# Optimization experiments

Hardware: AMD Instinct MI355X
Metric: run time of the kernel (lower is better)

The kernel has to match this reference:

```python
import jax, jax.numpy as jnp
import numpy as np

B, L, D, H = 4, 2048, 1024, 16
HD = D // H
EPS = 1e-5


def _layernorm(x, g, b):
    mu = jnp.mean(x, axis=-1, keepdims=True)
    var = jnp.mean(jnp.square(x - mu), axis=-1, keepdims=True)
    return (x - mu) * jax.lax.rsqrt(var + EPS) * g + b


def _rotate_half(x):
    x1, x2 = jnp.split(x, 2, axis=-1)
    return jnp.concatenate([-x2, x1], axis=-1)


def setup_inputs() -> dict:
    key = jax.random.key(0)
    ks = jax.random.split(key, 12)
    s = 0.02
    return {
        "x": jax.random.normal(ks[0], (B, L, D), jnp.float32),
        "pos_cos": jax.random.uniform(ks[1], (B, L, D), jnp.float32),
        "pos_sin": jax.random.uniform(ks[2], (B, L, D), jnp.float32),
        "attn_mask": jnp.zeros((B, L), jnp.float32),
        "Wq": jax.random.normal(ks[3], (D, D), jnp.float32) * s,
        "Wk": jax.random.normal(ks[4], (D, D), jnp.float32) * s,
        "Wv": jax.random.normal(ks[5], (D, D), jnp.float32) * s,
        "Wo": jax.random.normal(ks[6], (D, D), jnp.float32) * s,
        "W1": jax.random.normal(ks[7], (D, 2 * D), jnp.float32) * s,
        "W2": jax.random.normal(ks[8], (D, D), jnp.float32) * s,
        "g1": jnp.ones((D,), jnp.float32),
        "b1": jnp.zeros((D,), jnp.float32),
        "g2": jnp.ones((D,), jnp.float32),
        "b2": jnp.zeros((D,), jnp.float32),
    }


def reference(x, pos_cos, pos_sin, attn_mask, Wq, Wk, Wv, Wo, W1, W2, g1, b1, g2, b2):
    # --- attention sublayer (pre-LN) ---
    residual = x
    xn = _layernorm(x, g1, b1)
    split_heads = lambda t: t.reshape(B, L, H, HD).transpose(0, 2, 1, 3)  # [B,H,L,hd]
    q = split_heads(xn @ Wq)
    k = split_heads(xn @ Wk)
    v = split_heads(xn @ Wv)
    cos = split_heads(pos_cos)
    sin = split_heads(pos_sin)
    q = q * cos + _rotate_half(q) * sin
    k = k * cos + _rotate_half(k) * sin
    scores = jnp.einsum('bhqd,bhkd->bhqk', q, k) / np.float32(np.sqrt(HD))
    scores = scores + attn_mask[:, None, None, :]  # additive mask over keys
    probs = jax.nn.softmax(scores, axis=-1)
    ctx = jnp.einsum('bhqk,bhkd->bhqd', probs, v)
    ctx = ctx.transpose(0, 2, 1, 3).reshape(B, L, D)
    x = residual + ctx @ Wo
    # --- SwiGLU FFN sublayer (pre-LN) ---
    residual = x
    xn = _layernorm(x, g2, b2)
    h = xn @ W1
    x1, x2 = h[..., :D], h[..., D:]
    ffn = (jax.nn.silu(x1) * x2) @ W2
    return residual + ffn
```

## Files before the change

### kernel.cpp

```cpp
#include <hip/hip_runtime.h>
#include <hip/hip_bf16.h>

typedef unsigned short ushort_t;
typedef short short8 __attribute__((ext_vector_type(8)));
typedef unsigned short u16x4 __attribute__((ext_vector_type(4)));
typedef float f32x4 __attribute__((ext_vector_type(4)));
typedef int int2v __attribute__((ext_vector_type(2)));
typedef int int4v __attribute__((ext_vector_type(4)));

#define MFMA_BF16 __builtin_amdgcn_mfma_f32_16x16x32_bf16

#define GLDS16(g, l) __builtin_amdgcn_global_load_lds( \
    (__attribute__((address_space(1))) void*)(g), \
    (__attribute__((address_space(3))) void*)(l), 16, 0, 0)

__device__ __forceinline__ unsigned short f2bf(float f) {
  union { float f; unsigned u; } v; v.f = f;
  unsigned r = v.u + 0x7FFFu + ((v.u >> 16) & 1u);
  return (unsigned short)(r >> 16);
}
__device__ __forceinline__ float bf2f(unsigned short h) {
  union { unsigned u; float f; } v; v.u = ((unsigned)h) << 16;
  return v.f;
}
__device__ __forceinline__ unsigned pack_bf2(float a, float b) {
  __hip_bfloat162 t = __float22bfloat162_rn(float2{a, b});
  union { __hip_bfloat162 h; unsigned u; } v; v.h = t;
  return v.u;
}
__device__ __forceinline__ float exp2_raw(float x) {
  float r;
  asm volatile("v_exp_f32 %0, %1" : "=v"(r) : "v"(x));
  return r;
}

#define BB 4
#define LL 2048
#define DD 1024
#define HH 16
#define HD 64
#define NROW (BB * LL)
#define LOG2E 1.4426950408889634f

template <int PERM>
__global__ __launch_bounds__(256) void wconv(const float* __restrict__ W,
                                             ushort_t* __restrict__ WT,
                                             int R, int C) {
  __shared__ float tile[32][33];
  const int ct = blockIdx.x * 32, rt = blockIdx.y * 32;
  const int tx = threadIdx.x & 31, ty = threadIdx.x >> 5;
#pragma unroll
  for (int j = 0; j < 4; ++j)
    tile[ty + j * 8][tx] = W[(size_t)(rt + ty + j * 8) * C + ct + tx];
  __syncthreads();
  int orow0 = ct;
  if (PERM)
    orow0 = (ct < 1024) ? ((ct >> 5) * 64) : ((((ct - 1024) >> 5) * 64) + 32);
#pragma unroll
  for (int j = 0; j < 4; ++j)
    WT[(size_t)(orow0 + ty + j * 8) * R + rt + tx] = f2bf(tile[tx][ty + j * 8]);
}

__global__ void mask_scale(const float* __restrict__ mask,
                           float* __restrict__ maskl) {
  const int i = blockIdx.x * 256 + threadIdx.x;
  maskl[i] = mask[i] * LOG2E;
}

template <int BIN>
__global__ __launch_bounds__(256) void ln_kernel(const void* __restrict__ xin,
                                                 const float* __restrict__ g,
                                                 const float* __restrict__ bt,
                                                 ushort_t* __restrict__ out,
                                                 ushort_t* __restrict__ xb) {
  const int row = blockIdx.x, t = threadIdx.x;
  f32x4 v;
  if (BIN) {
    const u16x4 hv =
        *(const u16x4*)((const ushort_t*)xin + (size_t)row * DD + t * 4);
    v[0] = bf2f(hv[0]); v[1] = bf2f(hv[1]);
    v[2] = bf2f(hv[2]); v[3] = bf2f(hv[3]);
  } else {
    v = *(const f32x4*)((const float*)xin + (size_t)row * DD + t * 4);
    if (xb) {
      u16x4 xo;
      xo[0] = f2bf(v[0]); xo[1] = f2bf(v[1]);
      xo[2] = f2bf(v[2]); xo[3] = f2bf(v[3]);
      *(u16x4*)(xb + (size_t)row * DD + t * 4) = xo;
    }
  }
  float s = v[0] + v[1] + v[2] + v[3];
  float sq = v[0] * v[0] + v[1] * v[1] + v[2] * v[2] + v[3] * v[3];
#pragma unroll
  for (int off = 1; off < 64; off <<= 1) {
    s += __shfl_xor(s, off);
    sq += __shfl_xor(sq, off);
  }
  __shared__ float aw[4], aq[4];
  if ((t & 63) == 0) { aw[t >> 6] = s; aq[t >> 6] = sq; }
  __syncthreads();
  s = aw[0] + aw[1] + aw[2] + aw[3];
  sq = aq[0] + aq[1] + aq[2] + aq[3];
  const float mu = s * (1.f / DD);
  const float var = sq * (1.f / DD) - mu * mu;
  const float rs = rsqrtf(var + 1e-5f);
  u16x4 o;
#pragma unroll
  for (int j = 0; j < 4; ++j) {
    const int c = t * 4 + j;
    o[j] = f2bf((v[j] - mu) * rs * g[c] + bt[c]);
  }
  *(u16x4*)(out + (size_t)row * DD + t * 4) = o;
}

template <int EPI>
__global__ __launch_bounds__(256) void gemm64(
    const ushort_t* __restrict__ A, const ushort_t* __restrict__ BT,
    const float* __restrict__ pcos, const float* __restrict__ psin,
    ushort_t* __restrict__ qh, ushort_t* __restrict__ kh,
    ushort_t* __restrict__ vt, ushort_t* __restrict__ gact,
    ushort_t* __restrict__ Cb, float* __restrict__ Cf,
    const ushort_t* __restrict__ residb,
    int M, int N, int K) {
  __shared__ ushort_t As[2][128 * 64];
  __shared__ ushort_t Bs[2][128 * 64];
  const int tid = threadIdx.x;
  const int lane = tid & 63;
  const int w = tid >> 6;
  const int wr = w >> 1, wc = w & 1;
  const int orig = blockIdx.y * gridDim.x + blockIdx.x;
  const int xcd = orig & 7;
  const int lid = orig >> 3;
  const int bm = (xcd * 8 + (lid & 7)) * 128;
  const int bn = (lid >> 3) * 128;
  const int fr = lane & 15;
  const int hi = lane >> 4;
  const int srow8 = lane >> 3;
  const int schunk = (lane & 7) ^ srow8;
  f32x4 acc[4][4];
#pragma unroll
  for (int m = 0; m < 4; ++m)
#pragma unroll
    for (int n = 0; n < 4; ++n) acc[m][n] = (f32x4){0.f, 0.f, 0.f, 0.f};

#define STAGE64(kt, bb)                                                      \
  {                                                                          \
    _Pragma("unroll") for (int c = 0; c < 4; ++c) {                          \
      const int rbase = w * 32 + c * 8;                                      \
      const int grow = rbase + srow8;                                        \
      GLDS16(A + (size_t)(bm + grow) * K + (kt) * 64 + schunk * 8,           \
             &As[bb][rbase * 64]);                                           \
      GLDS16(BT + (size_t)(bn + grow) * K + (kt) * 64 + schunk * 8,          \
             &Bs[bb][rbase * 64]);                                           \
    }                                                                        \
  }

  const int nk = K >> 6;
  STAGE64(0, 0);
#pragma unroll 1
  for (int kt = 0; kt < nk; ++kt) {
    const int cur = kt & 1;
    if (kt + 1 < nk) {
      STAGE64(kt + 1, cur ^ 1);
      asm volatile("s_waitcnt vmcnt(8)" ::: "memory");
    } else {
      asm volatile("s_waitcnt vmcnt(0)" ::: "memory");
    }
    __syncthreads();
#pragma unroll
    for (int khf = 0; khf < 2; ++khf) {
      short8 af[4], bf_[4];
#pragma unroll
      for (int m = 0; m < 4; ++m) {
        const int r = wr * 64 + m * 16 + fr;
        af[m] =
            *(const short8*)&As[cur][r * 64 + (((khf << 2) + hi) ^ (fr & 7)) * 8];
      }
#pragma unroll
      for (int n = 0; n < 4; ++n) {
        const int r = wc * 64 + n * 16 + fr;
        bf_[n] =
            *(const short8*)&Bs[cur][r * 64 + (((khf << 2) + hi) ^ (fr & 7)) * 8];
      }
      __builtin_amdgcn_s_setprio(1);
#pragma unroll
      for (int m = 0; m < 4; ++m)
#pragma unroll
        for (int n = 0; n < 4; ++n)
          acc[m][n] = MFMA_BF16(af[m], bf_[n], acc[m][n], 0, 0, 0);
      __builtin_amdgcn_s_setprio(0);
    }
    __syncthreads();
  }
#undef STAGE64

  if (EPI == 1) {
    const int gcol = bn + wc * 64;
    const int region = gcol >> 10;
    const int h = (gcol & 1023) >> 6;
    const int b = bm >> 11;
    if (region < 2) {
      const float qs = (region == 0) ? (0.125f * LOG2E) : 1.0f;
      ushort_t* dstbuf = (region == 0) ? qh : kh;
      const int dbase = h * 64;
#pragma unroll
      for (int m = 0; m < 4; ++m) {
        const int gr0 = bm + wr * 64 + m * 16 + hi * 4;
#pragma unroll
        for (int r = 0; r < 4; ++r) {
          const int gr = gr0 + r;
          const int l = gr & 2047;
          const float* pcr = pcos + (size_t)gr * DD + dbase;
          const float* psr = psin + (size_t)gr * DD + dbase;
          ushort_t* dst = dstbuf + ((size_t)(b * HH + h) * LL + l) * HD;
#pragma unroll
          for (int n = 0; n < 2; ++n) {
            const int dlo = n * 16 + fr;
            const float xlo = acc[m][n][r], xhi = acc[m][n + 2][r];
            dst[dlo] = f2bf((xlo * pcr[dlo] - xhi * psr[dlo]) * qs);
            dst[dlo + 32] = f2bf((xhi * pcr[dlo + 32] + xlo * psr[dlo + 32]) * qs);
          }
        }
      }
    } else {
      const size_t bhv = (size_t)(b * HH + h);
      const int l0 = (bm & 2047) + wr * 64;
      const int lt = l0 >> 6;
#pragma unroll
      for (int m = 0; m < 4; ++m) {
        const int slotb = 32 * (m >> 1) + 8 * hi + 4 * (m & 1);
#pragma unroll
        for (int n = 0; n < 4; ++n) {
          const int hd = n * 16 + fr;
          u16x4 wv;
          wv[0] = f2bf(acc[m][n][0]);
          wv[1] = f2bf(acc[m][n][1]);
          wv[2] = f2bf(acc[m][n][2]);
          wv[3] = f2bf(acc[m][n][3]);
          *(u16x4*)(vt + (bhv * HD + hd) * LL + lt * 64 + slotb) = wv;
        }
      }
    }
  } else if (EPI == 2) {
    const int jbase = ((bn + wc * 64) >> 6) * 32;
#pragma unroll
    for (int m = 0; m < 4; ++m) {
      const int gr0 = bm + wr * 64 + m * 16 + hi * 4;
#pragma unroll
      for (int r = 0; r < 4; ++r) {
        ushort_t* dst = gact + (size_t)(gr0 + r) * DD + jbase;
#pragma unroll
        for (int n = 0; n < 2; ++n) {
          const float x1 = acc[m][n][r];
          const float x2 = acc[m][n + 2][r];
          dst[n * 16 + fr] = f2bf(x1 / (1.f + __expf(-x1)) * x2);
        }
      }
    }
  } else {
#pragma unroll
    for (int m = 0; m < 4; ++m)
#pragma unroll
      for (int n = 0; n < 4; ++n)
#pragma unroll
        for (int r = 0; r < 4; ++r) {
          const int gr = bm + wr * 64 + m * 16 + hi * 4 + r;
          const int gc = bn + wc * 64 + n * 16 + fr;
          const size_t o = (size_t)gr * N + gc;
          if (EPI == 3) Cb[o] = f2bf(bf2f(residb[o]) + acc[m][n][r]);
          else          Cf[o] = bf2f(residb[o]) + acc[m][n][r];
        }
  }
}

__global__ __launch_bounds__(512) void attn_kernel(
    const ushort_t* __restrict__ qh, const ushort_t* __restrict__ kh,
    const ushort_t* __restrict__ vt, const float* __restrict__ maskl,
    ushort_t* __restrict__ ctx) {
  const int tid = threadIdx.x, lane = tid & 63, w = tid >> 6;
  const int flat = blockIdx.y * gridDim.x + blockIdx.x;
  const int xcd = flat & 7;
  const int slot = flat >> 3;
  const int bh = xcd * 8 + (slot >> 4);
  const int q0 = (slot & 15) * 128;
  const int b = bh >> 4, h = bh & 15;
  __shared__ ushort_t Ks[2][64 * 64];
  __shared__ ushort_t Vs[2][64 * 64];
  const int fr = lane & 15;
  const int hi = lane >> 4;
  const int fo = hi * 8;
  const int qrow = q0 + w * 16 + fr;
  const size_t qoff = ((size_t)bh * LL + qrow) * HD + fo;
  const short8 qf0 = *(const short8*)(qh + qoff);
  const short8 qf1 = *(const short8*)(qh + qoff + 32);
  short8 ones;
#pragma unroll
  for (int i = 0; i < 8; ++i) ones[i] = (short)0x3F80;

  f32x4 oacc[4];
  f32x4 lacc = (f32x4){0.f, 0.f, 0.f, 0.f};
#pragma unroll
  for (int m = 0; m < 4; ++m) oacc[m] = (f32x4){0.f, 0.f, 0.f, 0.f};

  const int lrow = lane >> 3;
  const int lcs = ((lane & 7) ^ lrow) * 8;
  const int rr = w * 8 + lrow;

  const float* mrow = maskl + (size_t)b * LL;

  const int NT = LL / 128;
  for (int kt = 0; kt < NT; ++kt) {
    __syncthreads();
    GLDS16(kh + ((size_t)bh * LL + kt * 128 + rr) * HD + lcs, &Ks[0][w * 512]);
    GLDS16(kh + ((size_t)bh * LL + kt * 128 + 64 + rr) * HD + lcs,
           &Ks[1][w * 512]);
    GLDS16(vt + ((size_t)bh * HD + rr) * LL + kt * 128 + lcs, &Vs[0][w * 512]);
    GLDS16(vt + ((size_t)bh * HD + rr) * LL + kt * 128 + 64 + lcs,
           &Vs[1][w * 512]);
    f32x4 mk[8];
#pragma unroll
    for (int n = 0; n < 8; ++n)
      mk[n] = *(const f32x4*)(mrow + kt * 128 + n * 16 + hi * 4);
    asm volatile("s_waitcnt vmcnt(0)" ::: "memory");
    __syncthreads();

#pragma unroll
    for (int sub = 0; sub < 2; ++sub) {
      f32x4 s[4];
#pragma unroll
      for (int n = 0; n < 4; ++n) s[n] = mk[sub * 4 + n];
      __builtin_amdgcn_s_setprio(1);
#pragma unroll
      for (int n = 0; n < 4; ++n) {
        const int krow = n * 16 + fr;
#pragma unroll
        for (int c = 0; c < 2; ++c) {
          const int col = (c * 32 + fo) ^ ((fr & 7) * 8);
          const short8 kf = *(const short8*)&Ks[sub][krow * 64 + col];
          s[n] = MFMA_BF16(kf, c ? qf1 : qf0, s[n], 0, 0, 0);
        }
      }
      __builtin_amdgcn_s_setprio(0);
      unsigned pk[4][2];
#pragma unroll
      for (int n = 0; n < 4; ++n) {
        const float p0 = exp2_raw(s[n][0]);
        const float p1 = exp2_raw(s[n][1]);
        const float p2 = exp2_raw(s[n][2]);
        const float p3 = exp2_raw(s[n][3]);
        pk[n][0] = pack_bf2(p0, p1);
        pk[n][1] = pack_bf2(p2, p3);
      }
      __builtin_amdgcn_s_setprio(1);
#pragma unroll
      for (int c = 0; c < 2; ++c) {
        int4v pw = {(int)pk[2 * c][0], (int)pk[2 * c][1],
                    (int)pk[2 * c + 1][0], (int)pk[2 * c + 1][1]};
        union { int4v i; short8 s; } pf; pf.i = pw;
#pragma unroll
        for (int m = 0; m < 4; ++m) {
          const int row = m * 16 + fr;
          const int col = (c * 32 + fo) ^ ((fr & 7) * 8);
          const short8 vf = *(const short8*)&Vs[sub][row * 64 + col];
          oacc[m] = MFMA_BF16(vf, pf.s, oacc[m], 0, 0, 0);
        }
        lacc = MFMA_BF16(ones, pf.s, lacc, 0, 0, 0);
      }
      __builtin_amdgcn_s_setprio(0);
    }
  }
  const float inv = 1.f / lacc[0];
  const int q = q0 + w * 16 + fr;
  ushort_t* dst = ctx + ((size_t)b * LL + q) * DD + h * 64 + hi * 4;
#pragma unroll
  for (int m = 0; m < 4; ++m) {
    int2v val;
    val[0] = (int)pack_bf2(oacc[m][0] * inv, oacc[m][1] * inv);
    val[1] = (int)pack_bf2(oacc[m][2] * inv, oacc[m][3] * inv);
    *(int2v*)(dst + m * 16) = val;
  }
}

extern "C" void kernel_launch(void* const* d_in, const int* in_sizes, int n_in,
                              void* d_out, int out_size, void* d_ws,
                              size_t ws_size, hipStream_t stream) {
  const float* x = (const float*)d_in[0];
  const float* pcos = (const float*)d_in[1];
  const float* psin = (const float*)d_in[2];
  const float* mask = (const float*)d_in[3];
  const float* Wq = (const float*)d_in[4];
  const float* Wk = (const float*)d_in[5];
  const float* Wv = (const float*)d_in[6];
  const float* Wo = (const float*)d_in[7];
  const float* W1 = (const float*)d_in[8];
  const float* W2 = (const float*)d_in[9];
  const float* g1 = (const float*)d_in[10];
  const float* b1 = (const float*)d_in[11];
  const float* g2 = (const float*)d_in[12];
  const float* b2 = (const float*)d_in[13];
  float* out = (float*)d_out;
  char* ws = (char*)d_ws;

  ushort_t* WQKVT = (ushort_t*)(ws);
  ushort_t* WOT = (ushort_t*)(ws + 6291456);
  ushort_t* W1T = (ushort_t*)(ws + 8388608);
  ushort_t* W2T = (ushort_t*)(ws + 12582912);
  ushort_t* XN = (ushort_t*)(ws + 14680064);
  float* MASKL = (float*)(ws + 31457280);
  ushort_t* XB = (ushort_t*)(ws + 31457280 + 1048576);
  ushort_t* GACT = (ushort_t*)(ws + 31457280 + 33554432);
  ushort_t* QH = (ushort_t*)(ws + 81788928);
  ushort_t* KH = (ushort_t*)(ws + 98566144);
  ushort_t* VT = (ushort_t*)(ws + 115343360);
  ushort_t* CTX = (ushort_t*)(ws + 132120576);
  ushort_t* XMIDB = (ushort_t*)(ws + 148897792);

  wconv<0><<<dim3(32, 32), 256, 0, stream>>>(Wq, WQKVT, 1024, 1024);
  wconv<0><<<dim3(32, 32), 256, 0, stream>>>(Wk, WQKVT + 1024 * 1024, 1024, 1024);
  wconv<0><<<dim3(32, 32), 256, 0, stream>>>(Wv, WQKVT + 2 * 1024 * 1024, 1024, 1024);
  wconv<0><<<dim3(32, 32), 256, 0, stream>>>(Wo, WOT, 1024, 1024);
  wconv<1><<<dim3(64, 32), 256, 0, stream>>>(W1, W1T, 1024, 2048);
  wconv<0><<<dim3(32, 32), 256, 0, stream>>>(W2, W2T, 1024, 1024);
  mask_scale<<<(BB * LL) / 256, 256, 0, stream>>>(mask, MASKL);

  ln_kernel<0><<<NROW, 256, 0, stream>>>(x, g1, b1, XN, XB);
  gemm64<1><<<dim3(24, 64), 256, 0, stream>>>(
      XN, WQKVT, pcos, psin, QH, KH, VT, nullptr, nullptr, nullptr, nullptr,
      NROW, 3072, 1024);
  attn_kernel<<<dim3(16, 64), 512, 0, stream>>>(QH, KH, VT, MASKL, CTX);
  gemm64<3><<<dim3(8, 64), 256, 0, stream>>>(
      CTX, WOT, nullptr, nullptr, nullptr, nullptr, nullptr, nullptr, XMIDB,
      nullptr, XB, NROW, 1024, 1024);
  ln_kernel<1><<<NROW, 256, 0, stream>>>(XMIDB, g2, b2, XN, nullptr);
  gemm64<2><<<dim3(16, 64), 256, 0, stream>>>(
      XN, W1T, nullptr, nullptr, nullptr, nullptr, nullptr, GACT, nullptr,
      nullptr, nullptr, NROW, 2048, 1024);
  gemm64<4><<<dim3(8, 64), 256, 0, stream>>>(
      GACT, W2T, nullptr, nullptr, nullptr, nullptr, nullptr, nullptr, nullptr,
      out, XMIDB, NROW, 1024, 1024);
}
```

Measured before the change: 320.2 us.

## Add 256x256-tile GEMM kernel for QKV and W1 projections

```diff
diff --git a/kernel.cpp b/kernel.cpp
--- a/kernel.cpp
+++ b/kernel.cpp
@@ -116,12 +116,8 @@
 template <int EPI>
 __global__ __launch_bounds__(256) void gemm64(
     const ushort_t* __restrict__ A, const ushort_t* __restrict__ BT,
-    const float* __restrict__ pcos, const float* __restrict__ psin,
-    ushort_t* __restrict__ qh, ushort_t* __restrict__ kh,
-    ushort_t* __restrict__ vt, ushort_t* __restrict__ gact,
     ushort_t* __restrict__ Cb, float* __restrict__ Cf,
-    const ushort_t* __restrict__ residb,
-    int M, int N, int K) {
+    const ushort_t* __restrict__ residb, int M, int N, int K) {
   __shared__ ushort_t As[2][128 * 64];
   __shared__ ushort_t Bs[2][128 * 64];
   const int tid = threadIdx.x;
@@ -194,8 +190,101 @@
   }
 #undef STAGE64
 
+#pragma unroll
+  for (int m = 0; m < 4; ++m)
+#pragma unroll
+    for (int n = 0; n < 4; ++n)
+#pragma unroll
+      for (int r = 0; r < 4; ++r) {
+        const int gr = bm + wr * 64 + m * 16 + hi * 4 + r;
+        const int gc = bn + wc * 64 + n * 16 + fr;
+        const size_t o = (size_t)gr * N + gc;
+        if (EPI == 3) Cb[o] = f2bf(bf2f(residb[o]) + acc[m][n][r]);
+        else          Cf[o] = bf2f(residb[o]) + acc[m][n][r];
+      }
+}
+
+template <int EPI>
+__global__ __launch_bounds__(512, 1) void gemm256(
+    const ushort_t* __restrict__ A, const ushort_t* __restrict__ BT,
+    const float* __restrict__ pcos, const float* __restrict__ psin,
+    ushort_t* __restrict__ qh, ushort_t* __restrict__ kh,
+    ushort_t* __restrict__ vt, ushort_t* __restrict__ gact,
+    int M, int N, int K) {
+  __shared__ ushort_t As[2][256 * 64];
+  __shared__ ushort_t Bs[2][256 * 64];
+  const int tid = threadIdx.x;
+  const int lane = tid & 63;
+  const int w = tid >> 6;
+  const int wm = w >> 2, wn = w & 3;
+  const int orig = blockIdx.y * gridDim.x + blockIdx.x;
+  const int xcd = orig & 7;
+  const int lid = orig >> 3;
+  const int bm = (xcd * 4 + (lid & 3)) * 256;
+  const int bn = (lid >> 2) * 256;
+  const int fr = lane & 15;
+  const int hi = lane >> 4;
+  const int srow8 = lane >> 3;
+  const int schunk = (lane & 7) ^ srow8;
+  f32x4 acc[8][4];
+#pragma unroll
+  for (int m = 0; m < 8; ++m)
+#pragma unroll
+    for (int n = 0; n < 4; ++n) acc[m][n] = (f32x4){0.f, 0.f, 0.f, 0.f};
+
+#define STAGE256(kt, bb)                                                     \
+  {                                                                          \
+    _Pragma("unroll") for (int c = 0; c < 4; ++c) {                          \
+      const int rbase = w * 32 + c * 8;                                      \
+      const int grow = rbase + srow8;                                        \
+      GLDS16(A + (size_t)(bm + grow) * K + (kt) * 64 + schunk * 8,           \
+             &As[bb][rbase * 64]);                                           \
+      GLDS16(BT + (size_t)(bn + grow) * K + (kt) * 64 + schunk * 8,          \
+             &Bs[bb][rbase * 64]);                                           \
+    }                                                                        \
+  }
+
+  const int nk = K >> 6;
+  STAGE256(0, 0);
+#pragma unroll 1
+  for (int kt = 0; kt < nk; ++kt) {
+    const int cur = kt & 1;
+    if (kt + 1 < nk) {
+      STAGE256(kt + 1, cur ^ 1);
+      asm volatile("s_waitcnt vmcnt(8)" ::: "memory");
+    } else {
+      asm volatile("s_waitcnt vmcnt(0)" ::: "memory");
+    }
+    __syncthreads();
+#pragma unroll
+    for (int khf = 0; khf < 2; ++khf) {
+      short8 af[8], bf_[4];
+#pragma unroll
+      for (int m = 0; m < 8; ++m) {
+        const int r = wm * 128 + m * 16 + fr;
+        af[m] =
+            *(const short8*)&As[cur][r * 64 + (((khf << 2) + hi) ^ (fr & 7)) * 8];
+      }
+#pragma unroll
+      for (int n = 0; n < 4; ++n) {
+        const int r = wn * 64 + n * 16 + fr;
+        bf_[n] =
+            *(const short8*)&Bs[cur][r * 64 + (((khf << 2) + hi) ^ (fr & 7)) * 8];
+      }
+      __builtin_amdgcn_s_setprio(1);
+#pragma unroll
+      for (int m = 0; m < 8; ++m)
+#pragma unroll
+        for (int n = 0; n < 4; ++n)
+          acc[m][n] = MFMA_BF16(af[m], bf_[n], acc[m][n], 0, 0, 0);
+      __builtin_amdgcn_s_setprio(0);
+    }
+    __syncthreads();
+  }
+#undef STAGE256
+
   if (EPI == 1) {
-    const int gcol = bn + wc * 64;
+    const int gcol = bn + wn * 64;
     const int region = gcol >> 10;
     const int h = (gcol & 1023) >> 6;
     const int b = bm >> 11;
@@ -204,8 +293,8 @@
       ushort_t* dstbuf = (region == 0) ? qh : kh;
       const int dbase = h * 64;
 #pragma unroll
-      for (int m = 0; m < 4; ++m) {
-        const int gr0 = bm + wr * 64 + m * 16 + hi * 4;
+      for (int m = 0; m < 8; ++m) {
+        const int gr0 = bm + wm * 128 + m * 16 + hi * 4;
 #pragma unroll
         for (int r = 0; r < 4; ++r) {
           const int gr = gr0 + r;
@@ -224,11 +313,11 @@
       }
     } else {
       const size_t bhv = (size_t)(b * HH + h);
-      const int l0 = (bm & 2047) + wr * 64;
-      const int lt = l0 >> 6;
-#pragma unroll
-      for (int m = 0; m < 4; ++m) {
-        const int slotb = 32 * (m >> 1) + 8 * hi + 4 * (m & 1);
+#pragma unroll
+      for (int m = 0; m < 8; ++m) {
+        const int l0 = (bm & 2047) + wm * 128 + m * 16;
+        const int lt = l0 >> 6;
+        const int slotb = 32 * ((m >> 1) & 1) + 8 * hi + 4 * (m & 1);
 #pragma unroll
         for (int n = 0; n < 4; ++n) {
           const int hd = n * 16 + fr;
@@ -241,11 +330,11 @@
         }
       }
     }
-  } else if (EPI == 2) {
-    const int jbase = ((bn + wc * 64) >> 6) * 32;
-#pragma unroll
-    for (int m = 0; m < 4; ++m) {
-      const int gr0 = bm + wr * 64 + m * 16 + hi * 4;
+  } else {
+    const int jbase = ((bn + wn * 64) >> 6) * 32;
+#pragma unroll
+    for (int m = 0; m < 8; ++m) {
+      const int gr0 = bm + wm * 128 + m * 16 + hi * 4;
 #pragma unroll
       for (int r = 0; r < 4; ++r) {
         ushort_t* dst = gact + (size_t)(gr0 + r) * DD + jbase;
@@ -257,19 +346,6 @@
         }
       }
     }
-  } else {
-#pragma unroll
-    for (int m = 0; m < 4; ++m)
-#pragma unroll
-      for (int n = 0; n < 4; ++n)
-#pragma unroll
-        for (int r = 0; r < 4; ++r) {
-          const int gr = bm + wr * 64 + m * 16 + hi * 4 + r;
-          const int gc = bn + wc * 64 + n * 16 + fr;
-          const size_t o = (size_t)gr * N + gc;
-          if (EPI == 3) Cb[o] = f2bf(bf2f(residb[o]) + acc[m][n][r]);
-          else          Cf[o] = bf2f(residb[o]) + acc[m][n][r];
-        }
   }
 }
 
@@ -424,18 +500,15 @@
   mask_scale<<<(BB * LL) / 256, 256, 0, stream>>>(mask, MASKL);
 
   ln_kernel<0><<<NROW, 256, 0, stream>>>(x, g1, b1, XN, XB);
-  gemm64<1><<<dim3(24, 64), 256, 0, stream>>>(
-      XN, WQKVT, pcos, psin, QH, KH, VT, nullptr, nullptr, nullptr, nullptr,
-      NROW, 3072, 1024);
+  gemm256<1><<<dim3(12, 32), 512, 0, stream>>>(XN, WQKVT, pcos, psin, QH, KH,
+                                               VT, nullptr, NROW, 3072, 1024);
   attn_kernel<<<dim3(16, 64), 512, 0, stream>>>(QH, KH, VT, MASKL, CTX);
-  gemm64<3><<<dim3(8, 64), 256, 0, stream>>>(
-      CTX, WOT, nullptr, nullptr, nullptr, nullptr, nullptr, nullptr, XMIDB,
-      nullptr, XB, NROW, 1024, 1024);
+  gemm64<3><<<dim3(8, 64), 256, 0, stream>>>(CTX, WOT, XMIDB, nullptr, XB,
+                                             NROW, 1024, 1024);
   ln_kernel<1><<<NROW, 256, 0, stream>>>(XMIDB, g2, b2, XN, nullptr);
-  gemm64<2><<<dim3(16, 64), 256, 0, stream>>>(
-      XN, W1T, nullptr, nullptr, nullptr, nullptr, nullptr, GACT, nullptr,
-      nullptr, nullptr, NROW, 2048, 1024);
-  gemm64<4><<<dim3(8, 64), 256, 0, stream>>>(
-      GACT, W2T, nullptr, nullptr, nullptr, nullptr, nullptr, nullptr, nullptr,
-      out, XMIDB, NROW, 1024, 1024);
-}
+  gemm256<2><<<dim3(8, 32), 512, 0, stream>>>(XN, W1T, nullptr, nullptr,
+                                              nullptr, nullptr, nullptr, GACT,
+                                              NROW, 2048, 1024);
+  gemm64<4><<<dim3(8, 64), 256, 0, stream>>>(GACT, W2T, nullptr, out, XMIDB,
+                                             NROW, 1024, 1024);
+}
```

Measured after the change: 334.2 us. +4.4%, slower.
